# Optimization experiments

Hardware: AMD Instinct MI355X
Metric: run time of the kernel (lower is better)

Reference implementation:

```python
import jax, jax.numpy as jnp
import numpy as np

K = 3        # kernel_size
STRIDE = 1
PAD = 1
BASIS = 8    # act_fun.get_size()


def cheb_basis(x):
    """Chebyshev polynomial basis T_0..T_{BASIS-1} of tanh(x); appends basis axis."""
    t = jnp.tanh(x)
    polys = [jnp.ones_like(t), t]
    for _ in range(BASIS - 2):
        polys.append(2.0 * t * polys[-1] - polys[-2])
    return jnp.stack(polys, axis=-1)  # (..., BASIS)


def silu(x):
    return x * jax.nn.sigmoid(x)


def unfold(x):
    """torch F.unfold equivalent: (b,c,h,w) -> (b, c, K*K, L), L = ho*wo."""
    b, c, h, w = x.shape
    ho = (h - K + 2 * PAD) // STRIDE + 1
    wo = (w - K + 2 * PAD) // STRIDE + 1
    xp = jnp.pad(x, ((0, 0), (0, 0), (PAD, PAD), (PAD, PAD)))
    pats = [xp[:, :, i:i + STRIDE * ho:STRIDE, j:j + STRIDE * wo:STRIDE]
            for i in range(K) for j in range(K)]
    pats = jnp.stack(pats, axis=2)  # (b, c, K*K, ho, wo)
    return pats.reshape(b, c, K * K, ho * wo), ho, wo


def setup_inputs() -> dict:
    key = jax.random.key(0)
    k1, k2, k3 = jax.random.split(key, 3)
    cin, cout = 64, 64
    x = jax.random.normal(k1, (16, cin, 32, 32), dtype=jnp.float32)
    # xavier_normal_ on (in,out,k^2,1): std = sqrt(2/(fan_in+fan_out)) approx
    w = jax.random.normal(k2, (cin, cout, K * K), dtype=jnp.float32) * jnp.sqrt(2.0 / (cin + cout))
    # normal_(c, 0, 0.1) on (in,out,k^2,1,basis) -> squeeze the broadcast dim
    c = jax.random.normal(k3, (cin, cout, K * K, BASIS), dtype=jnp.float32) * 0.1
    return {"x": x, "w": w, "c": c}


def reference(x, w, c):
    b = x.shape[0]
    pats, ho, wo = unfold(x)          # (b, i, k, l)
    res = silu(pats)                  # residual activation path
    act = cheb_basis(pats)            # (b, i, k, l, s) spline basis
    # sum_i sum_k w[i,o,k] * res[b,i,k,l]
    term1 = jnp.einsum('iok,bikl->bol', w, res)
    # sum_i sum_k sum_s w[i,o,k]*c[i,o,k,s]*act[b,i,k,l,s] (fused, avoids (b,i,o,k,l,s))
    cw = c * w[..., None]             # (i, o, k, s)
    term2 = jnp.einsum('ioks,bikls->bol', cw, act)
    return (term1 + term2).reshape(b, -1, ho, wo)
```

## Files before the change

kernel.cpp:

```cpp
#include <hip/hip_runtime.h>
#include <hip/hip_bf16.h>


#define CIN   64
#define COUT  64
#define HW    32
#define LL    1024
#define NS    8

typedef __attribute__((ext_vector_type(8))) short short8;
typedef __attribute__((ext_vector_type(4))) float f32x4;


__global__ void prep_kernel(const float* __restrict__ w,
                            const float* __restrict__ c,
                            __hip_bfloat16* __restrict__ Wt,
                            float* __restrict__ bias) {
    int bx = blockIdx.x;
    if (bx >= 144) {
        const int o = bx - 144;
        const int i = threadIdx.x;
        if (i >= 64) return;
        float v = 0.f;
#pragma unroll
        for (int k = 0; k < 9; ++k) {
            const int idx = (i * COUT + o) * 9 + k;
            v += w[idx] * c[idx * 8];
        }
#pragma unroll
        for (int off = 32; off > 0; off >>= 1) v += __shfl_down(v, off);
        if (i == 0) bias[o] = v;
        return;
    }
    const int tid = bx * 256 + threadIdx.x;
    const int i = tid / (9 * COUT);
    const int r = tid - i * 9 * COUT;
    const int k = r / COUT;
    const int o = r - k * COUT;
    const int widx = (i * COUT + o) * 9 + k;
    const float wv = w[widx];
    __hip_bfloat16* dst = Wt + (size_t)tid * NS;
    dst[0] = __float2bfloat16(wv);
#pragma unroll
    for (int s = 1; s < 8; ++s) dst[s] = __float2bfloat16(wv * c[widx * 8 + s]);
}

__global__ __launch_bounds__(256, 4) void kan_fused_kernel(
        const float* __restrict__ x,
        const __hip_bfloat16* __restrict__ Wt,
        const float* __restrict__ bias,
        float* __restrict__ out) {
    __shared__ __align__(16) unsigned short Wlds[13056];

    const int tid   = threadIdx.x;
    const int wv    = tid >> 6;
    const int lane  = tid & 63;
    const int quad  = lane >> 4;
    const int l16   = lane & 15;

    const int b   = blockIdx.x;
    const int row = blockIdx.y;
    const int oh  = blockIdx.z;

    const unsigned short* WtU = (const unsigned short*)Wt;
    unsigned short* scratch = Wlds + wv * 3264;

    f32x4 acc[2][2];
#pragma unroll
    for (int h = 0; h < 2; ++h)
#pragma unroll
        for (int nt = 0; nt < 2; ++nt) acc[h][nt] = (f32x4){0.f, 0.f, 0.f, 0.f};

    for (int chunk = 0; chunk < 4; ++chunk) {
        const int chbase = wv * 16 + chunk * 4;
#pragma unroll
        for (int p = 0; p < 7; ++p) {
            const int cell = p * 64 + lane;
            if (cell < 408) {
                const int ch  = cell / 102;
                const int rem = cell - ch * 102;
                const int r3  = rem / 34;
                const int col = rem - r3 * 34;
                const int gy  = row - 1 + r3;
                const int gx  = col - 1;
                __align__(16) unsigned int u[4];
                if ((unsigned)gy < 32u && (unsigned)gx < 32u) {
                    const float xv = x[((size_t)(b * CIN + chbase + ch) * HW + gy) * HW + gx];
                    const float e   = __expf(-xv);
                    const float res = xv / (1.f + e);
                    const float e2  = __expf(2.f * xv);
                    const float t   = 1.f - 2.f / (e2 + 1.f);
                    const float T2 = 2.f * t * t  - 1.f;
                    const float T3 = 2.f * t * T2 - t;
                    const float T4 = 2.f * t * T3 - T2;
                    const float T5 = 2.f * t * T4 - T3;
                    const float T6 = 2.f * t * T5 - T4;
                    const float T7 = 2.f * t * T6 - T5;
                    __hip_bfloat16* hv = (__hip_bfloat16*)u;
                    hv[0] = __float2bfloat16(res); hv[1] = __float2bfloat16(t);
                    hv[2] = __float2bfloat16(T2);  hv[3] = __float2bfloat16(T3);
                    hv[4] = __float2bfloat16(T4);  hv[5] = __float2bfloat16(T5);
                    hv[6] = __float2bfloat16(T6);  hv[7] = __float2bfloat16(T7);
                } else {
                    u[0] = 0x00000000u; u[1] = 0x0000BF80u;
                    u[2] = 0x00003F80u; u[3] = 0x0000BF80u;
                }
                *(float4*)(scratch + cell * 8) = *(const float4*)u;
            }
        }

        const unsigned short* wchunk = WtU +
            ((size_t)(chbase + quad) * 9 * COUT + (oh << 5) + l16) * NS;
#pragma unroll
        for (int kpos = 0; kpos < 9; ++kpos) {
            const int dy = kpos / 3 - 1, dx = kpos % 3 - 1;
            const int cb = quad * 102 + (dy + 1) * 34 + (dx + 1);
            short8 af0 = *(const short8*)(scratch + (cb + l16) * 8);
            short8 af1 = *(const short8*)(scratch + (cb + 16 + l16) * 8);
#pragma unroll
            for (int nt = 0; nt < 2; ++nt) {
                short8 wf = *(const short8*)(wchunk + (kpos * COUT + nt * 16) * NS);
                acc[0][nt] = __builtin_amdgcn_mfma_f32_16x16x32_bf16(wf, af0, acc[0][nt], 0, 0, 0);
                acc[1][nt] = __builtin_amdgcn_mfma_f32_16x16x32_bf16(wf, af1, acc[1][nt], 0, 0, 0);
            }
        }
    }

    __syncthreads();
    float* red = (float*)Wlds;
#pragma unroll
    for (int h = 0; h < 2; ++h)
#pragma unroll
        for (int nt = 0; nt < 2; ++nt)
#pragma unroll
            for (int r = 0; r < 4; ++r) {
                const int p  = h * 16 + l16;
                const int ol = nt * 16 + quad * 4 + r;
                red[(wv * 32 + p) * 33 + ol] = acc[h][nt][r];
            }
    __syncthreads();

#pragma unroll
    for (int rep = 0; rep < 4; ++rep) {
        const int v  = rep * 256 + tid;
        const int p  = v & 31;
        const int ol = v >> 5;
        const int o  = (oh << 5) + ol;
        const float s = red[p * 33 + ol] + red[(32 + p) * 33 + ol]
                      + red[(64 + p) * 33 + ol] + red[(96 + p) * 33 + ol] + bias[o];
        out[(size_t)(b * COUT + o) * LL + row * HW + p] = s;
    }
}

extern "C" void kernel_launch(void* const* d_in, const int* in_sizes, int n_in,
                              void* d_out, int out_size, void* d_ws, size_t ws_size,
                              hipStream_t stream) {
    const float* x = (const float*)d_in[0];
    const float* w = (const float*)d_in[1];
    const float* c = (const float*)d_in[2];
    float* out = (float*)d_out;

    char* ws = (char*)d_ws;
    __hip_bfloat16* Wt   = (__hip_bfloat16*)(ws);
    float*          bias = (float*)(ws + 589824);

    prep_kernel<<<208, 256, 0, stream>>>(w, c, Wt, bias);
    kan_fused_kernel<<<dim3(16, 32, 2), 256, 0, stream>>>(x, Wt, bias, out);
}
```

Baseline: 85.81 us.

## Share basis computation across output halves in one 512-thread block with L2 prefetch

New measurement: 79.56 us. -7.3%, faster.

```diff
diff --git a/kernel.cpp b/kernel.cpp
--- a/kernel.cpp
+++ b/kernel.cpp
@@ -15,9 +15,25 @@
 __global__ void prep_kernel(const float* __restrict__ w,
                             const float* __restrict__ c,
                             __hip_bfloat16* __restrict__ Wt,
-                            float* __restrict__ bias) {
-    int bx = blockIdx.x;
-    if (bx >= 144) {
+                            float* __restrict__ bias,
+                            const float* __restrict__ x,
+                            float* __restrict__ dummy) {
+    const int bx = blockIdx.x;
+    if (bx < 144) {
+        const int tid = bx * 256 + threadIdx.x;
+        const int i = tid / (9 * COUT);
+        const int r = tid - i * 9 * COUT;
+        const int k = r / COUT;
+        const int o = r - k * COUT;
+        const int widx = (i * COUT + o) * 9 + k;
+        const float wv = w[widx];
+        __hip_bfloat16* dst = Wt + (size_t)tid * NS;
+        dst[0] = __float2bfloat16(wv);
+#pragma unroll
+        for (int s = 1; s < 8; ++s) dst[s] = __float2bfloat16(wv * c[widx * 8 + s]);
+        return;
+    }
+    if (bx < 208) {
         const int o = bx - 144;
         const int i = threadIdx.x;
         if (i >= 64) return;
@@ -32,38 +48,35 @@
         if (i == 0) bias[o] = v;
         return;
     }
-    const int tid = bx * 256 + threadIdx.x;
-    const int i = tid / (9 * COUT);
-    const int r = tid - i * 9 * COUT;
-    const int k = r / COUT;
-    const int o = r - k * COUT;
-    const int widx = (i * COUT + o) * 9 + k;
-    const float wv = w[widx];
-    __hip_bfloat16* dst = Wt + (size_t)tid * NS;
-    dst[0] = __float2bfloat16(wv);
-#pragma unroll
-    for (int s = 1; s < 8; ++s) dst[s] = __float2bfloat16(wv * c[widx * 8 + s]);
+    const int idx = bx - 208;
+    const int r  = idx & 7;
+    const int m  = idx >> 3;
+    const int b  = r + 8 * (m & 1);
+    const int ch = m >> 1;
+    const float4 v = ((const float4*)(x + (size_t)(b * CIN + ch) * LL))[threadIdx.x];
+    const float acc = v.x + v.y + v.z + v.w;
+    if (acc == 1.0e-37f) dummy[threadIdx.x] = acc;
 }
 
-__global__ __launch_bounds__(256, 4) void kan_fused_kernel(
+__global__ __launch_bounds__(512, 4) void kan_fused_kernel(
         const float* __restrict__ x,
         const __hip_bfloat16* __restrict__ Wt,
         const float* __restrict__ bias,
         float* __restrict__ out) {
-    __shared__ __align__(16) unsigned short Wlds[13056];
+    __shared__ __align__(16) unsigned short Wlds[26112];
 
     const int tid   = threadIdx.x;
     const int wv    = tid >> 6;
     const int lane  = tid & 63;
     const int quad  = lane >> 4;
     const int l16   = lane & 15;
+    const int kq    = wv >> 1;
+    const int oh    = wv & 1;
 
     const int b   = blockIdx.x;
     const int row = blockIdx.y;
-    const int oh  = blockIdx.z;
 
     const unsigned short* WtU = (const unsigned short*)Wt;
-    unsigned short* scratch = Wlds + wv * 3264;
 
     f32x4 acc[2][2];
 #pragma unroll
@@ -72,51 +85,54 @@
         for (int nt = 0; nt < 2; ++nt) acc[h][nt] = (f32x4){0.f, 0.f, 0.f, 0.f};
 
     for (int chunk = 0; chunk < 4; ++chunk) {
-        const int chbase = wv * 16 + chunk * 4;
+        const int chbase = kq * 16 + chunk * 4;
+        unsigned short* usd = Wlds + (chunk & 1) * 13056 + kq * 3264;
+
 #pragma unroll
-        for (int p = 0; p < 7; ++p) {
-            const int cell = p * 64 + lane;
+        for (int p = 0; p < 4; ++p) {
+            const int cell = (p * 2 + oh) * 64 + lane;
             if (cell < 408) {
-                const int ch  = cell / 102;
-                const int rem = cell - ch * 102;
-                const int r3  = rem / 34;
-                const int col = rem - r3 * 34;
+                const int ch  = cell & 3;
+                const int pos = cell >> 2;
+                const int r3  = (pos >= 68) ? 2 : ((pos >= 34) ? 1 : 0);
+                const int col = pos - r3 * 34;
                 const int gy  = row - 1 + r3;
                 const int gx  = col - 1;
-                __align__(16) unsigned int u[4];
+                union { __hip_bfloat162 h2[4]; float4 f4; unsigned int u[4]; } U;
                 if ((unsigned)gy < 32u && (unsigned)gx < 32u) {
                     const float xv = x[((size_t)(b * CIN + chbase + ch) * HW + gy) * HW + gx];
-                    const float e   = __expf(-xv);
-                    const float res = xv / (1.f + e);
+                    const float em  = __expf(-xv);
+                    const float res = xv * __builtin_amdgcn_rcpf(1.f + em);
                     const float e2  = __expf(2.f * xv);
-                    const float t   = 1.f - 2.f / (e2 + 1.f);
-                    const float T2 = 2.f * t * t  - 1.f;
-                    const float T3 = 2.f * t * T2 - t;
-                    const float T4 = 2.f * t * T3 - T2;
-                    const float T5 = 2.f * t * T4 - T3;
-                    const float T6 = 2.f * t * T5 - T4;
-                    const float T7 = 2.f * t * T6 - T5;
-                    __hip_bfloat16* hv = (__hip_bfloat16*)u;
-                    hv[0] = __float2bfloat16(res); hv[1] = __float2bfloat16(t);
-                    hv[2] = __float2bfloat16(T2);  hv[3] = __float2bfloat16(T3);
-                    hv[4] = __float2bfloat16(T4);  hv[5] = __float2bfloat16(T5);
-                    hv[6] = __float2bfloat16(T6);  hv[7] = __float2bfloat16(T7);
+                    const float t   = 1.f - 2.f * __builtin_amdgcn_rcpf(e2 + 1.f);
+                    const float t2  = t + t;
+                    const float T2 = __builtin_fmaf(t2, t,  -1.f);
+                    const float T3 = __builtin_fmaf(t2, T2, -t);
+                    const float T4 = __builtin_fmaf(t2, T3, -T2);
+                    const float T5 = __builtin_fmaf(t2, T4, -T3);
+                    const float T6 = __builtin_fmaf(t2, T5, -T4);
+                    const float T7 = __builtin_fmaf(t2, T6, -T5);
+                    U.h2[0] = __float22bfloat162_rn(make_float2(res, t));
+                    U.h2[1] = __float22bfloat162_rn(make_float2(T2, T3));
+                    U.h2[2] = __float22bfloat162_rn(make_float2(T4, T5));
+                    U.h2[3] = __float22bfloat162_rn(make_float2(T6, T7));
                 } else {
-                    u[0] = 0x00000000u; u[1] = 0x0000BF80u;
-                    u[2] = 0x00003F80u; u[3] = 0x0000BF80u;
+                    U.u[0] = 0x00000000u; U.u[1] = 0x0000BF80u;
+                    U.u[2] = 0x00003F80u; U.u[3] = 0x0000BF80u;
                 }
-                *(float4*)(scratch + cell * 8) = *(const float4*)u;
+                *(float4*)(usd + cell * 8) = U.f4;
             }
         }
+        __syncthreads();
 
         const unsigned short* wchunk = WtU +
             ((size_t)(chbase + quad) * 9 * COUT + (oh << 5) + l16) * NS;
 #pragma unroll
         for (int kpos = 0; kpos < 9; ++kpos) {
             const int dy = kpos / 3 - 1, dx = kpos % 3 - 1;
-            const int cb = quad * 102 + (dy + 1) * 34 + (dx + 1);
-            short8 af0 = *(const short8*)(scratch + (cb + l16) * 8);
-            short8 af1 = *(const short8*)(scratch + (cb + 16 + l16) * 8);
+            const int posb = (dy + 1) * 34 + (dx + 1);
+            short8 af0 = *(const short8*)(usd + ((posb + l16) * 4 + quad) * 8);
+            short8 af1 = *(const short8*)(usd + ((posb + 16 + l16) * 4 + quad) * 8);
 #pragma unroll
             for (int nt = 0; nt < 2; ++nt) {
                 short8 wf = *(const short8*)(wchunk + (kpos * COUT + nt * 16) * NS);
@@ -134,20 +150,19 @@
         for (int nt = 0; nt < 2; ++nt)
 #pragma unroll
             for (int r = 0; r < 4; ++r) {
-                const int p  = h * 16 + l16;
-                const int ol = nt * 16 + quad * 4 + r;
-                red[(wv * 32 + p) * 33 + ol] = acc[h][nt][r];
+                const int p = h * 16 + l16;
+                const int o = (oh << 5) + nt * 16 + quad * 4 + r;
+                red[(kq * 32 + p) * 65 + o] = acc[h][nt][r];
             }
     __syncthreads();
 
 #pragma unroll
     for (int rep = 0; rep < 4; ++rep) {
-        const int v  = rep * 256 + tid;
-        const int p  = v & 31;
-        const int ol = v >> 5;
-        const int o  = (oh << 5) + ol;
-        const float s = red[p * 33 + ol] + red[(32 + p) * 33 + ol]
-                      + red[(64 + p) * 33 + ol] + red[(96 + p) * 33 + ol] + bias[o];
+        const int v = rep * 512 + tid;
+        const int p = v & 31;
+        const int o = v >> 5;
+        const float s = red[p * 65 + o] + red[(32 + p) * 65 + o]
+                      + red[(64 + p) * 65 + o] + red[(96 + p) * 65 + o] + bias[o];
         out[(size_t)(b * COUT + o) * LL + row * HW + p] = s;
     }
 }
@@ -163,7 +178,8 @@
     char* ws = (char*)d_ws;
     __hip_bfloat16* Wt   = (__hip_bfloat16*)(ws);
     float*          bias = (float*)(ws + 589824);
+    float*          dummy = (float*)(ws + 590080);
 
-    prep_kernel<<<208, 256, 0, stream>>>(w, c, Wt, bias);
-    kan_fused_kernel<<<dim3(16, 32, 2), 256, 0, stream>>>(x, Wt, bias, out);
+    prep_kernel<<<1232, 256, 0, stream>>>(w, c, Wt, bias, x, dummy);
+    kan_fused_kernel<<<dim3(16, 32), 512, 0, stream>>>(x, Wt, bias, out);
 }
```
